# Optimization experiments

Measured on AMD Instinct MI355X. Metric: run time of the kernel, lower is better.

The kernel has to match this reference:

```python
import jax, jax.numpy as jnp
import numpy as np

B, J, M = 4, 2048, 4096   # batch, seq, d_model
N, D, K = 4, 16, 4096     # n adapters, lora rank, out dim


def setup_inputs() -> dict:
    key = jax.random.key(0)
    k1, k2, k3 = jax.random.split(key, 3)
    x = jax.random.normal(k1, (B, J, M), dtype=jnp.float32)
    lora_A = jax.random.normal(k2, (N, D, M), dtype=jnp.float32) * 0.02
    lora_B = jax.random.normal(k3, (N, K, D), dtype=jnp.float32) * 0.02
    return {"x": x, "lora_A": lora_A, "lora_B": lora_B}


def reference(x, lora_A, lora_B):
    # t[n,b,j,d] = x[b,j,m] @ lora_A[n,d,m]^T  (small-rank down-projection)
    t = jnp.einsum('bjm,ndm->nbjd', x, lora_A)
    # out[n,b,j,k] = t[n,b,j,d] @ lora_B[n,k,d]^T (up-projection)
    out = jnp.einsum('nbjd,nkd->nbjk', t, lora_B)
    return out
```

## Files before the change

kernel.cpp:

```cpp
#include <hip/hip_runtime.h>
#include <hip/hip_bf16.h>


#define MDIM 4096
#define KDIM 4096
#define RDIM 8192
#define NDND 64
#define MHALF 2048
#define TPART_STRIDE (4 * RDIM * 16)

__global__ __launch_bounds__(256) void lora_stage1(
    const float* __restrict__ x, const float* __restrict__ A,
    float* __restrict__ tpart) {
  const int tid = threadIdx.x;
  const int nd  = tid & 63;
  const int wv  = __builtin_amdgcn_readfirstlane(tid >> 6);
  const int rb  = blockIdx.x;
  const int mh  = blockIdx.y;
  const int row0 = rb * 32 + wv * 8;
  const int m0   = mh * MHALF;

  const float* Arow = A + (size_t)nd * MDIM + m0;
  const float* xr0  = x + (size_t)row0 * MDIM + m0;

  float acc[8];
#pragma unroll
  for (int r = 0; r < 8; ++r) acc[r] = 0.f;

#pragma unroll 2
  for (int m = 0; m < MHALF; m += 4) {
    const float4 a4 = *(const float4*)(Arow + m);
#pragma unroll
    for (int r = 0; r < 8; ++r) {
      const float4 xv = *(const float4*)(xr0 + (size_t)r * MDIM + m);
      acc[r] = fmaf(xv.w, a4.w,
               fmaf(xv.z, a4.z,
               fmaf(xv.y, a4.y,
               fmaf(xv.x, a4.x, acc[r]))));
    }
  }

  const int n = nd >> 4, d = nd & 15;
  float* tp = tpart + (size_t)mh * TPART_STRIDE;
#pragma unroll
  for (int r = 0; r < 8; ++r) {
    tp[((size_t)n * RDIM + (row0 + r)) * 16 + d] = acc[r];
  }
}

__global__ __launch_bounds__(256) void lora_stage2(
    const float* __restrict__ tpart, const float* __restrict__ Bm,
    float* __restrict__ out) {
  const int tid = threadIdx.x;
  const int kb  = blockIdx.x;
  const int n   = blockIdx.y;
  const int rc  = blockIdx.z;
  const int kk  = kb * 1024 + tid * 4;
  const int row0 = rc * 32;

  const float* Bn = Bm + ((size_t)n * KDIM + kk) * 16;
  float4 b[4][4];
#pragma unroll
  for (int i = 0; i < 4; ++i) {
#pragma unroll
    for (int q = 0; q < 4; ++q) {
      b[i][q] = *(const float4*)(Bn + i * 16 + q * 4);
    }
  }

  const float* t0 = tpart + ((size_t)n * RDIM + row0) * 16;
  const float* t1 = t0 + TPART_STRIDE;
  float* orow = out + ((size_t)n * RDIM + row0) * KDIM + kk;

  for (int r = 0; r < 32; ++r) {
    float4 tv[4];
#pragma unroll
    for (int q = 0; q < 4; ++q) {
      const float4 u = *(const float4*)(t0 + r * 16 + q * 4);
      const float4 v = *(const float4*)(t1 + r * 16 + q * 4);
      tv[q].x = u.x + v.x;
      tv[q].y = u.y + v.y;
      tv[q].z = u.z + v.z;
      tv[q].w = u.w + v.w;
    }
    float4 o;
    float* op = (float*)&o;
#pragma unroll
    for (int i = 0; i < 4; ++i) {
      float s = 0.f;
#pragma unroll
      for (int q = 0; q < 4; ++q) {
        s = fmaf(tv[q].x, b[i][q].x, s);
        s = fmaf(tv[q].y, b[i][q].y, s);
        s = fmaf(tv[q].z, b[i][q].z, s);
        s = fmaf(tv[q].w, b[i][q].w, s);
      }
      op[i] = s;
    }
    *(float4*)(orow + (size_t)r * KDIM) = o;
  }
}

extern "C" void kernel_launch(void* const* d_in, const int* in_sizes, int n_in,
                              void* d_out, int out_size, void* d_ws, size_t ws_size,
                              hipStream_t stream) {
  const float* x  = (const float*)d_in[0];
  const float* A  = (const float*)d_in[1];
  const float* Bm = (const float*)d_in[2];
  float* out   = (float*)d_out;
  float* tpart = (float*)d_ws;

  dim3 g1(256, 2, 1);
  lora_stage1<<<g1, 256, 0, stream>>>(x, A, tpart);

  dim3 g2(4, 4, 256);
  lora_stage2<<<g2, 256, 0, stream>>>(tpart, Bm, out);
}
```

Baseline: 947.2 us.

## Split stage-1 reduction into eight parts and stage t rows in LDS

```diff
diff --git a/kernel.cpp b/kernel.cpp
--- a/kernel.cpp
+++ b/kernel.cpp
@@ -1,13 +1,13 @@
 #include <hip/hip_runtime.h>
-#include <hip/hip_bf16.h>
 
 
 #define MDIM 4096
 #define KDIM 4096
 #define RDIM 8192
-#define NDND 64
-#define MHALF 2048
-#define TPART_STRIDE (4 * RDIM * 16)
+#define NADP 4
+#define NPARTS 8
+#define MPART (MDIM / NPARTS)
+#define TPART_FLOATS (NADP * RDIM * 16)
 
 __global__ __launch_bounds__(256) void lora_stage1(
     const float* __restrict__ x, const float* __restrict__ A,
@@ -18,7 +18,7 @@
   const int rb  = blockIdx.x;
   const int mh  = blockIdx.y;
   const int row0 = rb * 32 + wv * 8;
-  const int m0   = mh * MHALF;
+  const int m0   = mh * MPART;
 
   const float* Arow = A + (size_t)nd * MDIM + m0;
   const float* xr0  = x + (size_t)row0 * MDIM + m0;
@@ -27,8 +27,8 @@
 #pragma unroll
   for (int r = 0; r < 8; ++r) acc[r] = 0.f;
 
-#pragma unroll 2
-  for (int m = 0; m < MHALF; m += 4) {
+#pragma unroll 4
+  for (int m = 0; m < MPART; m += 4) {
     const float4 a4 = *(const float4*)(Arow + m);
 #pragma unroll
     for (int r = 0; r < 8; ++r) {
@@ -41,7 +41,7 @@
   }
 
   const int n = nd >> 4, d = nd & 15;
-  float* tp = tpart + (size_t)mh * TPART_STRIDE;
+  float* tp = tpart + (size_t)mh * TPART_FLOATS;
 #pragma unroll
   for (int r = 0; r < 8; ++r) {
     tp[((size_t)n * RDIM + (row0 + r)) * 16 + d] = acc[r];
@@ -51,12 +51,27 @@
 __global__ __launch_bounds__(256) void lora_stage2(
     const float* __restrict__ tpart, const float* __restrict__ Bm,
     float* __restrict__ out) {
+  __shared__ float4 tlds[512];
   const int tid = threadIdx.x;
   const int kb  = blockIdx.x;
   const int n   = blockIdx.y;
   const int rc  = blockIdx.z;
   const int kk  = kb * 1024 + tid * 4;
-  const int row0 = rc * 32;
+  const int row0 = rc * 128;
+
+  const float4* tp4 = (const float4*)tpart + ((size_t)n * RDIM + row0) * 4;
+  const size_t pstr4 = TPART_FLOATS / 4;
+#pragma unroll
+  for (int s0 = 0; s0 < 2; ++s0) {
+    const int s = tid + s0 * 256;
+    float4 sum = tp4[s];
+#pragma unroll
+    for (int p = 1; p < NPARTS; ++p) {
+      const float4 v = tp4[(size_t)p * pstr4 + s];
+      sum.x += v.x; sum.y += v.y; sum.z += v.z; sum.w += v.w;
+    }
+    tlds[s] = sum;
+  }
 
   const float* Bn = Bm + ((size_t)n * KDIM + kk) * 16;
   float4 b[4][4];
@@ -68,20 +83,15 @@
     }
   }
 
-  const float* t0 = tpart + ((size_t)n * RDIM + row0) * 16;
-  const float* t1 = t0 + TPART_STRIDE;
+  __syncthreads();
+
   float* orow = out + ((size_t)n * RDIM + row0) * KDIM + kk;
-
-  for (int r = 0; r < 32; ++r) {
+#pragma unroll 2
+  for (int r = 0; r < 128; ++r) {
     float4 tv[4];
 #pragma unroll
     for (int q = 0; q < 4; ++q) {
-      const float4 u = *(const float4*)(t0 + r * 16 + q * 4);
-      const float4 v = *(const float4*)(t1 + r * 16 + q * 4);
-      tv[q].x = u.x + v.x;
-      tv[q].y = u.y + v.y;
-      tv[q].z = u.z + v.z;
-      tv[q].w = u.w + v.w;
+      tv[q] = tlds[r * 4 + q];
     }
     float4 o;
     float* op = (float*)&o;
@@ -110,9 +120,9 @@
   float* out   = (float*)d_out;
   float* tpart = (float*)d_ws;
 
-  dim3 g1(256, 2, 1);
+  dim3 g1(256, NPARTS, 1);
   lora_stage1<<<g1, 256, 0, stream>>>(x, A, tpart);
 
-  dim3 g2(4, 4, 256);
+  dim3 g2(4, 4, 64);
   lora_stage2<<<g2, 256, 0, stream>>>(tpart, Bm, out);
 }
```

Result: faster. 898.7 us (-5.1%).
